# Performance work log

Hardware: AMD Instinct MI355X
Metric: run time of the kernel (lower is better)

The kernel has to match this reference:

```python
import jax, jax.numpy as jnp
import numpy as np

HEADS = 4


def setup_inputs() -> dict:
    key = jax.random.key(0)
    kx, kqkv, kbq, ko, kbo = jax.random.split(key, 5)
    B, C, H, W = 4, 256, 64, 64
    x = jax.random.normal(kx, (B, C, H, W), dtype=jnp.float32)
    # torch nn.Linear stores weight as [out_features, in_features]
    w_qkv = jax.random.normal(kqkv, (3 * C, C), dtype=jnp.float32) * (1.0 / np.sqrt(C))
    b_qkv = jax.random.normal(kbq, (3 * C,), dtype=jnp.float32) * 0.02
    w_o = jax.random.normal(ko, (C, C), dtype=jnp.float32) * (1.0 / np.sqrt(C))
    b_o = jax.random.normal(kbo, (C,), dtype=jnp.float32) * 0.02
    return {"x": x, "w_qkv": w_qkv, "b_qkv": b_qkv, "w_o": w_o, "b_o": b_o}


def reference(x, w_qkv, b_qkv, w_o, b_o):
    B, C, H, W = x.shape
    S = H * W
    hd = C // HEADS
    # (B, C, H, W) -> (B, S, C)
    xt = x.reshape(B, C, S).transpose(0, 2, 1)
    qkv = xt @ w_qkv.T + b_qkv                      # (B, S, 3C)
    q, k, v = jnp.split(qkv, 3, axis=-1)
    def to_heads(t):
        return t.reshape(B, S, HEADS, hd).transpose(0, 2, 1, 3)  # (B, h, S, hd)
    q, k, v = to_heads(q), to_heads(k), to_heads(v)
    scores = jnp.einsum('bhqd,bhkd->bhqk', q, k) / jnp.sqrt(jnp.float32(hd))
    attn = jax.nn.softmax(scores, axis=-1)          # dropout inactive (eval)
    out = jnp.einsum('bhqk,bhkd->bhqd', attn, v)    # (B, h, S, hd)
    out = out.transpose(0, 2, 1, 3).reshape(B, S, C)
    y = out @ w_o.T + b_o                            # (B, S, C)
    y = y.reshape(B, H, W, C).transpose(0, 3, 1, 2)  # (B, C, H, W)
    return y
```

## Files before the change

### kernel.cpp

```cpp
#include <hip/hip_runtime.h>
#include <stdint.h>

#define DI __device__ __forceinline__

typedef __attribute__((ext_vector_type(8))) __bf16 bf16x8;
typedef __attribute__((ext_vector_type(8))) unsigned short u16x8;
typedef __attribute__((ext_vector_type(4))) float f32x4;
typedef __attribute__((ext_vector_type(4))) uint32_t u32x4;
typedef __attribute__((ext_vector_type(4))) unsigned short u16x4;
typedef unsigned short u16;

constexpr int Bb = 4, Cc = 256, Ss = 4096, HD = 64;
constexpr int ELEMS = Bb * Cc * Ss;

DI u16 f2bf(float f) {
  union { float f; unsigned u; } x; x.f = f;
  return (u16)((x.u + 0x7FFFu + ((x.u >> 16) & 1u)) >> 16);
}
DI uint32_t pack2bf(float a, float b) {
  union { float f; uint32_t u; } xa, xb;
  xa.f = a; xb.f = b;
  return __builtin_amdgcn_perm(xb.u + 0x8000u, xa.u + 0x8000u, 0x07060302u);
}
DI bf16x8 ldfrag(const u16* p) { return __builtin_bit_cast(bf16x8, *(const u16x8*)p); }

__global__ __launch_bounds__(256) void k_convw(const float* __restrict__ w1, const float* __restrict__ w2,
                                               u16* __restrict__ d1, u16* __restrict__ d2) {
  int i = blockIdx.x * 256 + threadIdx.x;
  if (i < 196608) d1[i] = f2bf(w1[i]);
  if (i < 65536) d2[i] = f2bf(w2[i]);
}

__global__ __launch_bounds__(256) void k_transpose(const float* __restrict__ x, u16* __restrict__ xt) {
  __shared__ u16 T[64][72];
  const int st = blockIdx.x, ct = blockIdx.y, b = blockIdx.z;
  const int tid = threadIdx.x;
#pragma unroll
  for (int e = 0; e < 2; e++) {
    int ss = tid + e * 256;
    int r = ss >> 3, seg = ss & 7;
    size_t base = ((size_t)(b * Cc + ct * 64 + r) << 12) + st * 64 + seg * 8;
    u16x8 t;
#pragma unroll
    for (int j = 0; j < 8; j++) t[j] = f2bf(x[base + j]);
    *(u16x8*)&T[r][seg * 8] = t;
  }
  __syncthreads();
#pragma unroll
  for (int e = 0; e < 2; e++) {
    int ss = tid + e * 256;
    int sr = ss >> 3, cseg = ss & 7;
    u16x8 o;
#pragma unroll
    for (int j = 0; j < 8; j++) o[j] = T[cseg * 8 + j][sr];
    *(u16x8*)(xt + ((size_t)(b * Ss + st * 64 + sr) << 8) + ct * 64 + cseg * 8) = o;
  }
}

DI void stage_tile(const u16* __restrict__ src, int pitch, int r0, int k0, u16 (*dst)[40], int tid) {
#pragma unroll
  for (int e = 0; e < 2; e++) {
    int c = tid + e * 256;
    int row = c >> 2, seg = c & 3;
    u16x8 t = *(const u16x8*)(src + (size_t)(r0 + row) * pitch + k0 + seg * 8);
    *(u16x8*)&dst[row][seg * 8] = t;
  }
}

__global__ __launch_bounds__(256) void k_qkv(const u16* __restrict__ xt, const u16* __restrict__ w,
                                             const float* __restrict__ bias,
                                             u16* __restrict__ q, u16* __restrict__ kk_, u16* __restrict__ vv_) {
  __shared__ u16 As[128][40], Bs[128][40];
  const int tid = threadIdx.x;
  const int wv = tid >> 6, lane = tid & 63;
  const int wm = wv >> 1, wn = wv & 1;
  const int lr = lane & 15, quad = lane >> 4;
  const int r0 = blockIdx.x * 128;
  const int j0 = blockIdx.y * 128;
  f32x4 acc[4][4] = {};
  for (int k0 = 0; k0 < 256; k0 += 32) {
    __syncthreads();
    stage_tile(xt, 256, r0, k0, As, tid);
    stage_tile(w, 256, j0, k0, Bs, tid);
    __syncthreads();
    bf16x8 a[4], b[4];
#pragma unroll
    for (int mt = 0; mt < 4; mt++) a[mt] = ldfrag(&As[wm * 64 + mt * 16 + lr][quad * 8]);
#pragma unroll
    for (int nt = 0; nt < 4; nt++) b[nt] = ldfrag(&Bs[wn * 64 + nt * 16 + lr][quad * 8]);
#pragma unroll
    for (int mt = 0; mt < 4; mt++)
#pragma unroll
      for (int nt = 0; nt < 4; nt++)
        acc[mt][nt] = __builtin_amdgcn_mfma_f32_16x16x32_bf16(a[mt], b[nt], acc[mt][nt], 0, 0, 0);
  }
#pragma unroll
  for (int nt = 0; nt < 4; nt++) {
    int j = j0 + wn * 64 + nt * 16 + lr;
    float bj = bias[j];
    int part = j >> 8, cc = j & 255, head = cc >> 6, d = cc & 63;
    u16* outp = (part == 0) ? q : (part == 1) ? kk_ : vv_;
    float sc = (part == 0) ? 0.18033688f : 1.0f;
#pragma unroll
    for (int mt = 0; mt < 4; mt++)
#pragma unroll
      for (int rg = 0; rg < 4; rg++) {
        int row = r0 + wm * 64 + mt * 16 + quad * 4 + rg;
        int b_ = row >> 12, s = row & 4095;
        outp[((size_t)((b_ * 4 + head) * Ss + s) << 6) + d] = f2bf((acc[mt][nt][rg] + bj) * sc);
      }
  }
}

__global__ __launch_bounds__(256) void k_vt(const u16* __restrict__ v, u16* __restrict__ vt) {
  __shared__ u16 T[64][72];
  const int chunk = blockIdx.x, bh = blockIdx.y;
  const int tid = threadIdx.x;
#pragma unroll
  for (int e = 0; e < 2; e++) {
    int row = (tid >> 3) + e * 32, seg = tid & 7;
    *(u16x8*)&T[row][seg * 8] =
        *(const u16x8*)(v + ((size_t)(bh * Ss + chunk * 64 + row) << 6) + seg * 8);
  }
  __syncthreads();
#pragma unroll
  for (int e = 0; e < 2; e++) {
    int d = (tid >> 3) + e * 32, seg = tid & 7;
    u16x8 o;
#pragma unroll
    for (int j = 0; j < 8; j++) {
      int slot = seg * 8 + j;
      int t = (((slot >> 5) & 1) << 1) | ((slot >> 2) & 1);
      int w6 = t * 16 + (((slot >> 3) & 3) << 2) + (slot & 3);
      o[j] = T[w6][d];
    }
    *(u16x8*)(vt + ((size_t)(bh * 64 + d) << 12) + chunk * 64 + seg * 8) = o;
  }
}

__global__ __launch_bounds__(256, 2) void k_attn(const u16* __restrict__ Q, const u16* __restrict__ K,
                                                 const u16* __restrict__ VT, u16* __restrict__ AO,
                                                 float* __restrict__ Opart, float* __restrict__ lpart,
                                                 int nsplit) {
  __shared__ u16 Kl[2][64][72];
  __shared__ u16 Vl[2][64][72];
  const int tid = threadIdx.x;
  const int wv = tid >> 6, lane = tid & 63;
  const int lr = lane & 15, quad = lane >> 4;
  const int bh = blockIdx.y;
  const int b_ = bh >> 2, head = bh & 3;
  const int qbase = blockIdx.x * 256 + wv * 64;
  const int sp = blockIdx.z;
  const int nchunk = 64 / nsplit, kcg0 = sp * nchunk;
  const u16* Qh = Q + (size_t)bh * Ss * HD;
  const u16* Kh = K + (size_t)bh * Ss * HD;
  const u16* Vh = VT + (size_t)bh * HD * Ss;

  bf16x8 qb[4][2];
#pragma unroll
  for (int nt = 0; nt < 4; nt++)
#pragma unroll
    for (int ks = 0; ks < 2; ks++)
      qb[nt][ks] = ldfrag(Qh + (size_t)(qbase + nt * 16 + lr) * HD + ks * 32 + quad * 8);

  f32x4 O[4][4] = {};
  float lsum[4] = {0.f, 0.f, 0.f, 0.f};

  u16x8 pf[4];
  const int srow = tid >> 3, sseg = tid & 7;
  auto load_chunk = [&](int kc) {
#pragma unroll
    for (int e = 0; e < 2; e++) {
      pf[e] = *(const u16x8*)(Kh + ((size_t)((kcg0 + kc) * 64 + srow + e * 32) << 6) + sseg * 8);
      pf[2 + e] = *(const u16x8*)(Vh + ((size_t)(srow + e * 32) << 12) + (kcg0 + kc) * 64 + sseg * 8);
    }
  };
  auto store_chunk = [&](int buf) {
#pragma unroll
    for (int e = 0; e < 2; e++) {
      *(u16x8*)&Kl[buf][srow + e * 32][sseg * 8] = pf[e];
      *(u16x8*)&Vl[buf][srow + e * 32][sseg * 8] = pf[2 + e];
    }
  };

  load_chunk(0);
  store_chunk(0);
  if (nchunk > 1) load_chunk(1);
  __syncthreads();

  for (int kc = 0; kc < nchunk; kc++) {
    const int cur = kc & 1;
    f32x4 St[4][4] = {};
#pragma unroll
    for (int ks = 0; ks < 2; ks++) {
      bf16x8 ka[4];
#pragma unroll
      for (int kt = 0; kt < 4; kt++) ka[kt] = ldfrag(&Kl[cur][kt * 16 + lr][ks * 32 + quad * 8]);
#pragma unroll
      for (int kt = 0; kt < 4; kt++)
#pragma unroll
        for (int nt = 0; nt < 4; nt++)
          St[kt][nt] = __builtin_amdgcn_mfma_f32_16x16x32_bf16(ka[kt], qb[nt][ks], St[kt][nt], 0, 0, 0);
    }

    uint32_t pk[4][4][2];
#pragma unroll
    for (int kt = 0; kt < 4; kt++)
#pragma unroll
      for (int nt = 0; nt < 4; nt++) {
        float p0 = __builtin_amdgcn_exp2f(St[kt][nt][0]);
        float p1 = __builtin_amdgcn_exp2f(St[kt][nt][1]);
        float p2 = __builtin_amdgcn_exp2f(St[kt][nt][2]);
        float p3 = __builtin_amdgcn_exp2f(St[kt][nt][3]);
        lsum[nt] += (p0 + p1) + (p2 + p3);
        pk[kt][nt][0] = pack2bf(p0, p1);
        pk[kt][nt][1] = pack2bf(p2, p3);
      }

#pragma unroll
    for (int ks = 0; ks < 2; ks++) {
      bf16x8 pa[4];
#pragma unroll
      for (int mt = 0; mt < 4; mt++) {
        u32x4 t = {pk[2 * ks][mt][0], pk[2 * ks][mt][1], pk[2 * ks + 1][mt][0], pk[2 * ks + 1][mt][1]};
        pa[mt] = __builtin_bit_cast(bf16x8, t);
      }
#pragma unroll
      for (int dt = 0; dt < 4; dt++) {
        bf16x8 vb = ldfrag(&Vl[cur][dt * 16 + lr][ks * 32 + quad * 8]);
#pragma unroll
        for (int mt = 0; mt < 4; mt++)
          O[mt][dt] = __builtin_amdgcn_mfma_f32_16x16x32_bf16(pa[mt], vb, O[mt][dt], 0, 0, 0);
      }
    }

    if (kc + 1 < nchunk) {
      store_chunk(cur ^ 1);
      if (kc + 2 < nchunk) load_chunk(kc + 2);
    }
    __syncthreads();
  }

#pragma unroll
  for (int nt = 0; nt < 4; nt++) {
    lsum[nt] += __shfl_xor(lsum[nt], 16);
    lsum[nt] += __shfl_xor(lsum[nt], 32);
  }

  if (nsplit == 1) {
#pragma unroll
    for (int mt = 0; mt < 4; mt++)
#pragma unroll
      for (int rg = 0; rg < 4; rg++) {
        float lv = __shfl(lsum[mt], quad * 4 + rg);
        float inv = 1.0f / lv;
        int s = qbase + mt * 16 + quad * 4 + rg;
#pragma unroll
        for (int dt = 0; dt < 4; dt++)
          AO[((size_t)(b_ * Ss + s) << 8) + head * 64 + dt * 16 + lr] = f2bf(O[mt][dt][rg] * inv);
      }
  } else {
    float* Op = Opart + (size_t)sp * ELEMS;
    float* lp = lpart + (size_t)sp * (16 * Ss) + bh * Ss;
    if (quad == 0) {
#pragma unroll
      for (int nt = 0; nt < 4; nt++) lp[qbase + nt * 16 + lr] = lsum[nt];
    }
#pragma unroll
    for (int mt = 0; mt < 4; mt++)
#pragma unroll
      for (int rg = 0; rg < 4; rg++) {
        int s = qbase + mt * 16 + quad * 4 + rg;
#pragma unroll
        for (int dt = 0; dt < 4; dt++)
          Op[((size_t)(b_ * Ss + s) << 8) + head * 64 + dt * 16 + lr] = O[mt][dt][rg];
      }
  }
}

__global__ __launch_bounds__(256) void k_comb(const float* __restrict__ Opart, const float* __restrict__ lpart,
                                              u16* __restrict__ ao, int nsplit) {
  int idx = (blockIdx.x * 256 + threadIdx.x) * 4;
  int c = idx & 255, bs = idx >> 8;
  int b = bs >> 12, s = bs & 4095, head = c >> 6;
  int li = (b * 4 + head) * Ss + s;
  f32x4 oacc = *(const f32x4*)(Opart + idx);
  float l = lpart[li];
  for (int j = 1; j < nsplit; j++) {
    f32x4 oj = *(const f32x4*)(Opart + (size_t)j * ELEMS + idx);
#pragma unroll
    for (int t = 0; t < 4; t++) oacc[t] += oj[t];
    l += lpart[(size_t)j * 16 * Ss + li];
  }
  float inv = 1.0f / l;
  u16x4 o;
#pragma unroll
  for (int j = 0; j < 4; j++) o[j] = f2bf(oacc[j] * inv);
  *(u16x4*)(ao + idx) = o;
}

__global__ __launch_bounds__(256) void k_oproj(const u16* __restrict__ wo, const u16* __restrict__ ao,
                                               const float* __restrict__ bo, float* __restrict__ y) {
  __shared__ u16 As[128][40], Bs[128][40];
  const int tid = threadIdx.x;
  const int wv = tid >> 6, lane = tid & 63;
  const int wm = wv >> 1, wn = wv & 1;
  const int lr = lane & 15, quad = lane >> 4;
  const int c0 = blockIdx.x * 128;
  const int n0 = blockIdx.y * 128;
  f32x4 acc[4][4] = {};
  for (int k0 = 0; k0 < 256; k0 += 32) {
    __syncthreads();
    stage_tile(wo, 256, c0, k0, As, tid);
    stage_tile(ao, 256, n0, k0, Bs, tid);
    __syncthreads();
    bf16x8 a[4], b[4];
#pragma unroll
    for (int mt = 0; mt < 4; mt++) a[mt] = ldfrag(&As[wm * 64 + mt * 16 + lr][quad * 8]);
#pragma unroll
    for (int nt = 0; nt < 4; nt++) b[nt] = ldfrag(&Bs[wn * 64 + nt * 16 + lr][quad * 8]);
#pragma unroll
    for (int mt = 0; mt < 4; mt++)
#pragma unroll
      for (int nt = 0; nt < 4; nt++)
        acc[mt][nt] = __builtin_amdgcn_mfma_f32_16x16x32_bf16(a[mt], b[nt], acc[mt][nt], 0, 0, 0);
  }
#pragma unroll
  for (int mt = 0; mt < 4; mt++)
#pragma unroll
    for (int rg = 0; rg < 4; rg++) {
      int c = c0 + wm * 64 + mt * 16 + quad * 4 + rg;
      float bc = bo[c];
#pragma unroll
      for (int nt = 0; nt < 4; nt++) {
        int col = n0 + wn * 64 + nt * 16 + lr;
        int b_ = col >> 12, s = col & 4095;
        y[((size_t)(b_ * Cc + c) << 12) + s] = acc[mt][nt][rg] + bc;
      }
    }
}

extern "C" void kernel_launch(void* const* d_in, const int* in_sizes, int n_in,
                              void* d_out, int out_size, void* d_ws, size_t ws_size,
                              hipStream_t stream) {
  const float* x = (const float*)d_in[0];
  const float* w_qkv = (const float*)d_in[1];
  const float* b_qkv = (const float*)d_in[2];
  const float* w_o = (const float*)d_in[3];
  const float* b_o = (const float*)d_in[4];
  float* y = (float*)d_out;
  u16* ws = (u16*)d_ws;
  u16* xt = ws;
  u16* q = ws + (size_t)ELEMS;
  u16* k = ws + (size_t)2 * ELEMS;
  u16* vt = ws + (size_t)3 * ELEMS;
  u16* ao = xt;
  u16* wqb = ws + (size_t)4 * ELEMS;
  u16* wob = wqb + 196608;
  const size_t Wu16 = (size_t)4 * ELEMS + 262144;
  float* Opart = (float*)(ws + Wu16);
  u16* v = (u16*)Opart;
  const size_t base = Wu16 * 2;
  auto need = [&](int n) { return base + (size_t)n * ELEMS * 4 + (size_t)n * 16 * Ss * 4; };
  const int nsplit = (ws_size >= need(4)) ? 4 : (ws_size >= need(2)) ? 2 : 1;
  float* lpart = Opart + (size_t)nsplit * ELEMS;

  k_convw<<<768, 256, 0, stream>>>(w_qkv, w_o, wqb, wob);
  k_transpose<<<dim3(64, 4, 4), 256, 0, stream>>>(x, xt);
  k_qkv<<<dim3(128, 6), 256, 0, stream>>>(xt, wqb, b_qkv, q, k, v);
  k_vt<<<dim3(64, 16), 256, 0, stream>>>(v, vt);
  k_attn<<<dim3(16, 16, nsplit), 256, 0, stream>>>(q, k, vt, ao, Opart, lpart, nsplit);
  if (nsplit > 1) k_comb<<<ELEMS / 1024, 256, 0, stream>>>(Opart, lpart, ao, nsplit);
  k_oproj<<<dim3(2, 128), 256, 0, stream>>>(wob, ao, b_o, y);
}
```

Before: 198.3 us.

## Fuse split-combine into output projection, compute row sums via MFMA, reduce splits

The split-K combine kernel is removed and its work is folded into the output-projection B-tile staging, so partial outputs are summed and normalised on the fly. The projection now uses 512-thread blocks covering all 256 output channels. In attention, the per-lane softmax row sums are replaced by an extra MFMA against a ones vector, P is packed to bf16 by truncation instead of rounding, and the next chunk's LDS store and load are moved to the start of each iteration. The key split count drops from 4 to 2. Truncation changes numerics slightly, and the fewer splits lower attention grid parallelism.

Result: faster. 184.7 us (-6.9%).

```diff
diff --git a/kernel.cpp b/kernel.cpp
--- a/kernel.cpp
+++ b/kernel.cpp
@@ -7,7 +7,6 @@
 typedef __attribute__((ext_vector_type(8))) unsigned short u16x8;
 typedef __attribute__((ext_vector_type(4))) float f32x4;
 typedef __attribute__((ext_vector_type(4))) uint32_t u32x4;
-typedef __attribute__((ext_vector_type(4))) unsigned short u16x4;
 typedef unsigned short u16;
 
 constexpr int Bb = 4, Cc = 256, Ss = 4096, HD = 64;
@@ -17,10 +16,10 @@
   union { float f; unsigned u; } x; x.f = f;
   return (u16)((x.u + 0x7FFFu + ((x.u >> 16) & 1u)) >> 16);
 }
-DI uint32_t pack2bf(float a, float b) {
+DI uint32_t pack2bf_trunc(float a, float b) {
   union { float f; uint32_t u; } xa, xb;
   xa.f = a; xb.f = b;
-  return __builtin_amdgcn_perm(xb.u + 0x8000u, xa.u + 0x8000u, 0x07060302u);
+  return __builtin_amdgcn_perm(xb.u, xa.u, 0x07060302u);
 }
 DI bf16x8 ldfrag(const u16* p) { return __builtin_bit_cast(bf16x8, *(const u16x8*)p); }
 
@@ -163,8 +162,13 @@
     for (int ks = 0; ks < 2; ks++)
       qb[nt][ks] = ldfrag(Qh + (size_t)(qbase + nt * 16 + lr) * HD + ks * 32 + quad * 8);
 
+  u16x8 ov;
+#pragma unroll
+  for (int j = 0; j < 8; j++) ov[j] = 0x3F80;
+  const bf16x8 ones = __builtin_bit_cast(bf16x8, ov);
+
   f32x4 O[4][4] = {};
-  float lsum[4] = {0.f, 0.f, 0.f, 0.f};
+  f32x4 lacc[4] = {};
 
   u16x8 pf[4];
   const int srow = tid >> 3, sseg = tid & 7;
@@ -190,6 +194,11 @@
 
   for (int kc = 0; kc < nchunk; kc++) {
     const int cur = kc & 1;
+    if (kc + 1 < nchunk) {
+      store_chunk(cur ^ 1);
+      if (kc + 2 < nchunk) load_chunk(kc + 2);
+    }
+
     f32x4 St[4][4] = {};
 #pragma unroll
     for (int ks = 0; ks < 2; ks++) {
@@ -212,9 +221,8 @@
         float p1 = __builtin_amdgcn_exp2f(St[kt][nt][1]);
         float p2 = __builtin_amdgcn_exp2f(St[kt][nt][2]);
         float p3 = __builtin_amdgcn_exp2f(St[kt][nt][3]);
-        lsum[nt] += (p0 + p1) + (p2 + p3);
-        pk[kt][nt][0] = pack2bf(p0, p1);
-        pk[kt][nt][1] = pack2bf(p2, p3);
+        pk[kt][nt][0] = pack2bf_trunc(p0, p1);
+        pk[kt][nt][1] = pack2bf_trunc(p2, p3);
       }
 
 #pragma unroll
@@ -232,19 +240,12 @@
         for (int mt = 0; mt < 4; mt++)
           O[mt][dt] = __builtin_amdgcn_mfma_f32_16x16x32_bf16(pa[mt], vb, O[mt][dt], 0, 0, 0);
       }
-    }
-
-    if (kc + 1 < nchunk) {
-      store_chunk(cur ^ 1);
-      if (kc + 2 < nchunk) load_chunk(kc + 2);
-    }
-    __syncthreads();
-  }
-
-#pragma unroll
-  for (int nt = 0; nt < 4; nt++) {
-    lsum[nt] += __shfl_xor(lsum[nt], 16);
-    lsum[nt] += __shfl_xor(lsum[nt], 32);
+#pragma unroll
+      for (int mt = 0; mt < 4; mt++)
+        lacc[mt] = __builtin_amdgcn_mfma_f32_16x16x32_bf16(pa[mt], ones, lacc[mt], 0, 0, 0);
+    }
+
+    __syncthreads();
   }
 
   if (nsplit == 1) {
@@ -252,8 +253,7 @@
     for (int mt = 0; mt < 4; mt++)
 #pragma unroll
       for (int rg = 0; rg < 4; rg++) {
-        float lv = __shfl(lsum[mt], quad * 4 + rg);
-        float inv = 1.0f / lv;
+        float inv = 1.0f / lacc[mt][rg];
         int s = qbase + mt * 16 + quad * 4 + rg;
 #pragma unroll
         for (int dt = 0; dt < 4; dt++)
@@ -262,9 +262,11 @@
   } else {
     float* Op = Opart + (size_t)sp * ELEMS;
     float* lp = lpart + (size_t)sp * (16 * Ss) + bh * Ss;
-    if (quad == 0) {
-#pragma unroll
-      for (int nt = 0; nt < 4; nt++) lp[qbase + nt * 16 + lr] = lsum[nt];
+    if (lr == 0) {
+#pragma unroll
+      for (int mt = 0; mt < 4; mt++)
+#pragma unroll
+        for (int rg = 0; rg < 4; rg++) lp[qbase + mt * 16 + quad * 4 + rg] = lacc[mt][rg];
     }
 #pragma unroll
     for (int mt = 0; mt < 4; mt++)
@@ -278,41 +280,49 @@
   }
 }
 
-__global__ __launch_bounds__(256) void k_comb(const float* __restrict__ Opart, const float* __restrict__ lpart,
-                                              u16* __restrict__ ao, int nsplit) {
-  int idx = (blockIdx.x * 256 + threadIdx.x) * 4;
-  int c = idx & 255, bs = idx >> 8;
-  int b = bs >> 12, s = bs & 4095, head = c >> 6;
-  int li = (b * 4 + head) * Ss + s;
-  f32x4 oacc = *(const f32x4*)(Opart + idx);
-  float l = lpart[li];
-  for (int j = 1; j < nsplit; j++) {
-    f32x4 oj = *(const f32x4*)(Opart + (size_t)j * ELEMS + idx);
-#pragma unroll
-    for (int t = 0; t < 4; t++) oacc[t] += oj[t];
-    l += lpart[(size_t)j * 16 * Ss + li];
-  }
-  float inv = 1.0f / l;
-  u16x4 o;
-#pragma unroll
-  for (int j = 0; j < 4; j++) o[j] = f2bf(oacc[j] * inv);
-  *(u16x4*)(ao + idx) = o;
-}
-
-__global__ __launch_bounds__(256) void k_oproj(const u16* __restrict__ wo, const u16* __restrict__ ao,
-                                               const float* __restrict__ bo, float* __restrict__ y) {
-  __shared__ u16 As[128][40], Bs[128][40];
+__global__ __launch_bounds__(512) void k_oproj(const u16* __restrict__ wo, const u16* __restrict__ ao,
+                                               const float* __restrict__ Opart, const float* __restrict__ lpart,
+                                               const float* __restrict__ bo, float* __restrict__ y, int nsplit) {
+  __shared__ u16 As[256][40], Bs[128][40];
   const int tid = threadIdx.x;
   const int wv = tid >> 6, lane = tid & 63;
   const int wm = wv >> 1, wn = wv & 1;
   const int lr = lane & 15, quad = lane >> 4;
-  const int c0 = blockIdx.x * 128;
-  const int n0 = blockIdx.y * 128;
+  const int n0 = blockIdx.x * 128;
   f32x4 acc[4][4] = {};
   for (int k0 = 0; k0 < 256; k0 += 32) {
     __syncthreads();
-    stage_tile(wo, 256, c0, k0, As, tid);
-    stage_tile(ao, 256, n0, k0, Bs, tid);
+#pragma unroll
+    for (int e = 0; e < 2; e++) {
+      int c = tid + e * 512;
+      int row = c >> 2, seg = c & 3;
+      *(u16x8*)&As[row][seg * 8] = *(const u16x8*)(wo + row * 256 + k0 + seg * 8);
+    }
+    {
+      int c = tid;
+      int row = c >> 2, seg = c & 3;
+      int bs = n0 + row, cc = k0 + seg * 8;
+      u16x8 t;
+      if (nsplit == 1) {
+        t = *(const u16x8*)(ao + ((size_t)bs << 8) + cc);
+      } else {
+        int b = bs >> 12, s = bs & 4095, head = cc >> 6;
+        int li = (b * 4 + head) * Ss + s;
+        f32x4 o0 = {}, o1 = {};
+        float l = 0.f;
+        for (int j = 0; j < nsplit; j++) {
+          const float* Op = Opart + (size_t)j * ELEMS + ((size_t)bs << 8) + cc;
+          f32x4 a0 = *(const f32x4*)Op, a1 = *(const f32x4*)(Op + 4);
+#pragma unroll
+          for (int i = 0; i < 4; i++) { o0[i] += a0[i]; o1[i] += a1[i]; }
+          l += lpart[(size_t)j * 16 * Ss + li];
+        }
+        float inv = 1.0f / l;
+#pragma unroll
+        for (int i = 0; i < 4; i++) { t[i] = f2bf(o0[i] * inv); t[4 + i] = f2bf(o1[i] * inv); }
+      }
+      *(u16x8*)&Bs[row][seg * 8] = t;
+    }
     __syncthreads();
     bf16x8 a[4], b[4];
 #pragma unroll
@@ -329,7 +339,7 @@
   for (int mt = 0; mt < 4; mt++)
 #pragma unroll
     for (int rg = 0; rg < 4; rg++) {
-      int c = c0 + wm * 64 + mt * 16 + quad * 4 + rg;
+      int c = wm * 64 + mt * 16 + quad * 4 + rg;
       float bc = bo[c];
 #pragma unroll
       for (int nt = 0; nt < 4; nt++) {
@@ -362,7 +372,7 @@
   u16* v = (u16*)Opart;
   const size_t base = Wu16 * 2;
   auto need = [&](int n) { return base + (size_t)n * ELEMS * 4 + (size_t)n * 16 * Ss * 4; };
-  const int nsplit = (ws_size >= need(4)) ? 4 : (ws_size >= need(2)) ? 2 : 1;
+  const int nsplit = (ws_size >= need(2)) ? 2 : 1;
   float* lpart = Opart + (size_t)nsplit * ELEMS;
 
   k_convw<<<768, 256, 0, stream>>>(w_qkv, w_o, wqb, wob);
@@ -370,6 +380,5 @@
   k_qkv<<<dim3(128, 6), 256, 0, stream>>>(xt, wqb, b_qkv, q, k, v);
   k_vt<<<dim3(64, 16), 256, 0, stream>>>(v, vt);
   k_attn<<<dim3(16, 16, nsplit), 256, 0, stream>>>(q, k, vt, ao, Opart, lpart, nsplit);
-  if (nsplit > 1) k_comb<<<ELEMS / 1024, 256, 0, stream>>>(Opart, lpart, ao, nsplit);
-  k_oproj<<<dim3(2, 128), 256, 0, stream>>>(wob, ao, b_o, y);
-}
+  k_oproj<<<128, 512, 0, stream>>>(wob, ao, Opart, lpart, b_o, y, nsplit);
+}
```
